# Kernel optimization log

Hardware: AMD Instinct MI355X
Metric: run time of the kernel (lower is better)

The kernel has to match this reference:

```python
import jax, jax.numpy as jnp
import numpy as np


def _euclidean_cdist(x, q):
    # torch.cdist with p=2: pairwise L2 distances, shape [B, Q]
    x2 = jnp.sum(x * x, axis=-1, keepdims=True)          # [B, 1]
    q2 = jnp.sum(q * q, axis=-1)[None, :]                # [1, Q]
    d2 = x2 + q2 - 2.0 * (x @ q.T)                        # [B, Q]
    return jnp.sqrt(jnp.maximum(d2, 0.0))


def setup_inputs() -> dict:
    key = jax.random.key(0)
    k1, k2 = jax.random.split(key)
    x = jax.random.normal(k1, (1024, 256), dtype=jnp.float32)
    queue = jax.random.normal(k2, (32768, 256), dtype=jnp.float32)
    return {"x": x, "queue": queue}


def reference(x, queue):
    # Queue update: concat then keep the newest max_size rows (queue assumed full)
    max_size = queue.shape[0]
    q = jnp.concatenate([queue, x], axis=0)[-max_size:]   # [Q, F]
    # Distance matrix + top-2 nearest (topk of negated distances)
    d = _euclidean_cdist(x, q)                            # [B, Q]
    _, idx = jax.lax.top_k(-d, 2)                         # [B, 2]
    # Second-nearest neighbor (first is the point itself, dist 0)
    return q[idx[:, 1]]                                   # [B, F]
```

## Files before the change

### kernel.cpp

```cpp
#include <hip/hip_runtime.h>
#include <stdint.h>

#define B_ROWS 1024
#define FEAT   256
#define QSZ    32768
#define SHIFT  1024
#define QX     (QSZ - B_ROWS)
#define BM     64
#define NGY    (QSZ / BM)
#define NCOL   1024
#define MARGIN 8.0f

typedef float  v4f __attribute__((ext_vector_type(4)));
typedef short  v8s __attribute__((ext_vector_type(8)));
typedef int    v4i __attribute__((ext_vector_type(4)));

#define PIN8(X)                                        \
    {                                                  \
        v4i _t = __builtin_bit_cast(v4i, X);           \
        asm volatile("" : "+v"(_t));                   \
        X = __builtin_bit_cast(v8s, _t);               \
    }

__device__ __forceinline__ uint32_t key_flip(uint32_t u) {
    return u ^ ((uint32_t)((int32_t)u >> 31) | 0x80000000u);
}
__device__ __forceinline__ float key_m(uint32_t k) {
    uint32_t u = k & 0xFFFF8000u;
    u = (u & 0x80000000u) ? (u ^ 0x80000000u) : ~u;
    return __uint_as_float(u);
}
__device__ __forceinline__ void k2_insert(uint32_t& k1, uint32_t& k2, uint32_t key) {
    uint32_t hi = max(k1, key); k1 = min(k1, key); k2 = min(k2, hi);
}
__device__ __forceinline__ uint2 k2_merge(uint2 a, uint2 b) {
    uint32_t hi = max(a.x, b.x);
    uint2 r; r.x = min(a.x, b.x); r.y = min(min(a.y, b.y), hi);
    return r;
}

struct Top2 { float m1; int j1; float m2; int j2; };
__device__ __forceinline__ bool better(float ma, int ja, float mb, int jb) {
    return (ma < mb) || (ma == mb && ja < jb);
}
__device__ __forceinline__ void t2_insert(Top2& t, float m, int j) {
    if (better(m, j, t.m1, t.j1)) { t.m2 = t.m1; t.j2 = t.j1; t.m1 = m; t.j1 = j; }
    else if (better(m, j, t.m2, t.j2)) { t.m2 = m; t.j2 = j; }
}

__device__ __forceinline__ const float* q_row_ptr(int j, const float* x, const float* queue) {
    return (j < QX) ? (queue + (size_t)(j + SHIFT) * FEAT) : (x + (size_t)(j - QX) * FEAT);
}

__device__ __forceinline__ unsigned short f2bf(float f) {
    uint32_t u = __float_as_uint(f);
    uint32_t r = u + 0x7FFFu + ((u >> 16) & 1u);
    return (unsigned short)(r >> 16);
}

__global__ __launch_bounds__(256) void convert_x(const float* __restrict__ x,
                                                 unsigned short* __restrict__ x_bf) {
    int wave = threadIdx.x >> 6, lane = threadIdx.x & 63;
    int r = blockIdx.x * 4 + wave;
    float4 v = ((const float4*)(x + (size_t)r * FEAT))[lane];
    ushort4 h;
    h.x = f2bf(v.x); h.y = f2bf(v.y); h.z = f2bf(v.z); h.w = f2bf(v.w);
    ((ushort4*)x_bf)[(size_t)r * 64 + lane] = h;
}


#define KEYI(ACC, Q2V, J)                                                  \
    {                                                                      \
        float m_ = fmaf(-2.0f, (ACC), (Q2V));                              \
        uint32_t u_ = key_flip(__float_as_uint(m_));                       \
        k2_insert(k1, k2, (u_ & 0xFFFF8000u) | (uint32_t)(J));             \
    }

#define PROCESS(TN, FB)                                                    \
    {                                                                      \
        v4f a0 = (v4f)0.0f, a1 = (v4f)0.0f, a2 = (v4f)0.0f, a3 = (v4f)0.0f;\
        __builtin_amdgcn_s_setprio(1);                                     \
        _Pragma("unroll")                                                  \
        for (int kc = 0; kc < 8; ++kc) {                                   \
            a0 = __builtin_amdgcn_mfma_f32_16x16x32_bf16(fa0[kc], FB[kc], a0, 0, 0, 0); \
            a1 = __builtin_amdgcn_mfma_f32_16x16x32_bf16(fa1[kc], FB[kc], a1, 0, 0, 0); \
            a2 = __builtin_amdgcn_mfma_f32_16x16x32_bf16(fa2[kc], FB[kc], a2, 0, 0, 0); \
            a3 = __builtin_amdgcn_mfma_f32_16x16x32_bf16(fa3[kc], FB[kc], a3, 0, 0, 0); \
        }                                                                  \
        __builtin_amdgcn_s_setprio(0);                                     \
        uint32_t k1 = 0xFFFFFFFFu, k2 = 0xFFFFFFFFu;                       \
        _Pragma("unroll")                                                  \
        for (int r = 0; r < 4; ++r) {                                      \
            KEYI(a0[r], q2r0[r], jb + 0  + r);                             \
            KEYI(a1[r], q2r1[r], jb + 16 + r);                             \
            KEYI(a2[r], q2r2[r], jb + 32 + r);                             \
            KEYI(a3[r], q2r3[r], jb + 48 + r);                             \
        }                                                                  \
        _Pragma("unroll")                                                  \
        for (int mask = 16; mask <= 32; mask <<= 1) {                      \
            uint32_t o1 = __shfl_xor(k1, mask, 64);                        \
            uint32_t o2 = __shfl_xor(k2, mask, 64);                        \
            uint32_t hi = max(k1, o1);                                     \
            k1 = min(k1, o1);                                              \
            k2 = min(min(k2, o2), hi);                                     \
        }                                                                  \
        if (quad == 0)                                                     \
            partials[(size_t)gy * NCOL + (w * 256 + (TN) * 16 + l16)] =    \
                make_uint2(k1, k2);                                        \
    }

__global__ __launch_bounds__(256, 2) void nn_gemm(const float* __restrict__ x,
                                                  const float* __restrict__ queue,
                                                  const unsigned short* __restrict__ x_bf,
                                                  float* __restrict__ q2,
                                                  uint2* __restrict__ partials) {
    __shared__ __align__(16) unsigned short As[BM * FEAT];
    __shared__ __align__(16) float sq2[BM];

    const int t    = threadIdx.x;
    const int w    = t >> 6, lane = t & 63;
    const int quad = lane >> 4, l16 = lane & 15;
    const int gy   = blockIdx.x;

    const unsigned short* bbase = x_bf + (size_t)(w * 256 + l16) * FEAT + quad * 8;
    v8s fb0[8], fb1[8];
#pragma unroll
    for (int kc = 0; kc < 8; ++kc) fb0[kc] = *(const v8s*)(bbase + kc * 32);

    {
        const int arow = t >> 2, aqtr = t & 3;
        const float* asrc = q_row_ptr(gy * BM + arow, x, queue) + aqtr * 64;
        float ss = 0.0f;
#pragma unroll
        for (int gi = 0; gi < 8; ++gi) {
            float4 a = *(const float4*)(asrc + gi * 8);
            float4 b = *(const float4*)(asrc + gi * 8 + 4);
            ss += a.x * a.x + a.y * a.y + a.z * a.z + a.w * a.w
                + b.x * b.x + b.y * b.y + b.z * b.z + b.w * b.w;
            uint32_t p0 = (uint32_t)f2bf(a.x) | ((uint32_t)f2bf(a.y) << 16);
            uint32_t p1 = (uint32_t)f2bf(a.z) | ((uint32_t)f2bf(a.w) << 16);
            uint32_t p2 = (uint32_t)f2bf(b.x) | ((uint32_t)f2bf(b.y) << 16);
            uint32_t p3 = (uint32_t)f2bf(b.z) | ((uint32_t)f2bf(b.w) << 16);
            const int g    = aqtr * 8 + gi;
            const int phys = (g & 24) | ((g & 7) ^ (arow & 7));
            *(uint4*)&As[arow * FEAT + phys * 8] = make_uint4(p0, p1, p2, p3);
        }
        ss += __shfl_xor(ss, 1, 64);
        ss += __shfl_xor(ss, 2, 64);
        if (aqtr == 0) { sq2[arow] = ss; q2[gy * BM + arow] = ss; }
    }

    __syncthreads();

    v8s fa0[8], fa1[8], fa2[8], fa3[8];
#pragma unroll
    for (int kc = 0; kc < 8; ++kc) {
        const int g  = kc * 4 + quad;
        const int pg = (g & 24) | ((g & 7) ^ (l16 & 7));
        const char* rowb = (const char*)As + (size_t)l16 * 512 + pg * 16;
        fa0[kc] = *(const v8s*)(rowb);
        fa1[kc] = *(const v8s*)(rowb + 1 * 16 * 512);
        fa2[kc] = *(const v8s*)(rowb + 2 * 16 * 512);
        fa3[kc] = *(const v8s*)(rowb + 3 * 16 * 512);
    }
#pragma unroll
    for (int kc = 0; kc < 8; ++kc) {
        PIN8(fa0[kc]); PIN8(fa1[kc]); PIN8(fa2[kc]); PIN8(fa3[kc]);
    }

    v4f q2r0 = *(const v4f*)&sq2[ 0 + quad * 4];
    v4f q2r1 = *(const v4f*)&sq2[16 + quad * 4];
    v4f q2r2 = *(const v4f*)&sq2[32 + quad * 4];
    v4f q2r3 = *(const v4f*)&sq2[48 + quad * 4];
    const int jb = gy * BM + quad * 4;

#pragma unroll
    for (int tp = 0; tp < 8; ++tp) {
        const int tn0 = tp * 2;
#pragma unroll
        for (int kc = 0; kc < 8; ++kc)
            fb1[kc] = *(const v8s*)(bbase + (size_t)(tn0 + 1) * (16 * FEAT) + kc * 32);
        PROCESS(tn0, fb0);
        if (tp < 7) {
#pragma unroll
            for (int kc = 0; kc < 8; ++kc)
                fb0[kc] = *(const v8s*)(bbase + (size_t)(tn0 + 2) * (16 * FEAT) + kc * 32);
        }
        PROCESS(tn0 + 1, fb1);
    }
}

__global__ __launch_bounds__(256) void nn_finalize(const float* __restrict__ x,
                                                   const float* __restrict__ queue,
                                                   const float* __restrict__ q2,
                                                   const uint2* __restrict__ partials,
                                                   float* __restrict__ out) {
    __shared__ float    xs[256];
    __shared__ uint2    red[256];
    __shared__ int      list[64];
    __shared__ float    escore[64];
    __shared__ int      s_cnt;
    __shared__ uint32_t s_kcut;
    __shared__ int      s_j2;

    const int t = threadIdx.x, i = blockIdx.x;
    const int w = t >> 6, lane = t & 63;

    xs[t] = x[(size_t)i * FEAT + t];
    uint2 pa = partials[(size_t)t * NCOL + i];
    uint2 pb = partials[(size_t)(t + 256) * NCOL + i];
    uint2 pm = k2_merge(pa, pb);
    red[t] = pm;
    if (t == 0) s_cnt = 0;
    __syncthreads();

    if (w == 0) {
        uint2 a = red[lane];
        a = k2_merge(a, red[lane + 64]);
        a = k2_merge(a, red[lane + 128]);
        a = k2_merge(a, red[lane + 192]);
#pragma unroll
        for (int mask = 1; mask <= 32; mask <<= 1) {
            uint2 o;
            o.x = __shfl_xor(a.x, mask, 64);
            o.y = __shfl_xor(a.y, mask, 64);
            a = k2_merge(a, o);
        }
        if (lane == 0) {
            float cutf = key_m(a.y) + MARGIN;
            s_kcut = key_flip(__float_as_uint(cutf)) | 0x7FFFu;
        }
    }
    __syncthreads();
    uint32_t kcut = s_kcut;
    if (pm.x <= kcut) { int q_ = atomicAdd(&s_cnt, 1); if (q_ < 64) list[q_] = (int)(pm.x & 0x7FFFu); }
    if (pm.y <= kcut) { int q_ = atomicAdd(&s_cnt, 1); if (q_ < 64) list[q_] = (int)(pm.y & 0x7FFFu); }
    __syncthreads();
    int n = min(s_cnt, 64);

    for (int c = w; c < n; c += 4) {
        int j = list[c];
        const float4* qr = (const float4*)q_row_ptr(j, x, queue);
        float4 qv = qr[lane];
        float4 xv = ((const float4*)xs)[lane];
        float s = qv.x * xv.x + qv.y * xv.y + qv.z * xv.z + qv.w * xv.w;
#pragma unroll
        for (int off = 32; off; off >>= 1) s += __shfl_xor(s, off, 64);
        if (lane == 0) escore[c] = q2[j] - 2.0f * s;
    }
    __syncthreads();
    if (t == 0) {
        Top2 a;
        a.m1 = __builtin_inff(); a.j1 = 0x7FFFFFFF;
        a.m2 = __builtin_inff(); a.j2 = 0x7FFFFFFF;
        for (int c = 0; c < n; ++c) t2_insert(a, escore[c], list[c]);
        s_j2 = a.j2;
    }
    __syncthreads();
    out[(size_t)i * FEAT + t] = q_row_ptr(s_j2, x, queue)[t];
}

extern "C" void kernel_launch(void* const* d_in, const int* in_sizes, int n_in,
                              void* d_out, int out_size, void* d_ws, size_t ws_size,
                              hipStream_t stream) {
    const float* x     = (const float*)d_in[0];
    const float* queue = (const float*)d_in[1];

    unsigned short* x_bf     = (unsigned short*)d_ws;
    float*          q2       = (float*)((char*)d_ws + (1u << 20));
    uint2*          partials = (uint2*)((char*)d_ws + (2u << 20));

    convert_x<<<B_ROWS / 4, 256, 0, stream>>>(x, x_bf);
    nn_gemm<<<NGY, 256, 0, stream>>>(x, queue, x_bf, q2, partials);
    nn_finalize<<<B_ROWS, 256, 0, stream>>>(x, queue, q2, partials, (float*)d_out);
}
```

Baseline: 122.0 us.

## Pre-convert whole queue to bf16 in separate pass, load A fragments from global

The queue (plus x) conversion to bf16 and its squared-norm computation move out of the GEMM kernel into a standalone convert pass over all 32768 rows. The GEMM then reads bf16 A fragments and norms directly from global memory with no LDS staging or block barrier. The partials layout is also transposed so the finalize kernel reads each query's 512 candidates contiguously. The cost is an extra 16 MB bf16 write plus re-read, in exchange for a simpler, barrier-free GEMM prologue and coalesced finalize loads.

New measurement: 128.7 us. 5.5% more time.

```diff
diff --git a/kernel.cpp b/kernel.cpp
--- a/kernel.cpp
+++ b/kernel.cpp
@@ -58,14 +58,21 @@
     return (unsigned short)(r >> 16);
 }
 
-__global__ __launch_bounds__(256) void convert_x(const float* __restrict__ x,
-                                                 unsigned short* __restrict__ x_bf) {
+__global__ __launch_bounds__(256) void convert_kernel(const float* __restrict__ x,
+                                                      const float* __restrict__ queue,
+                                                      unsigned short* __restrict__ q_bf,
+                                                      float* __restrict__ q2) {
     int wave = threadIdx.x >> 6, lane = threadIdx.x & 63;
-    int r = blockIdx.x * 4 + wave;
-    float4 v = ((const float4*)(x + (size_t)r * FEAT))[lane];
+    int j = blockIdx.x * 4 + wave;
+    const float4* row = (const float4*)q_row_ptr(j, x, queue);
+    float4 v = row[lane];
+    float s = v.x * v.x + v.y * v.y + v.z * v.z + v.w * v.w;
+#pragma unroll
+    for (int off = 32; off; off >>= 1) s += __shfl_xor(s, off, 64);
+    if (lane == 0) q2[j] = s;
     ushort4 h;
     h.x = f2bf(v.x); h.y = f2bf(v.y); h.z = f2bf(v.z); h.w = f2bf(v.w);
-    ((ushort4*)x_bf)[(size_t)r * 64 + lane] = h;
+    ((ushort4*)q_bf)[(size_t)j * 64 + lane] = h;
 }
 
 
@@ -105,73 +112,42 @@
             k2 = min(min(k2, o2), hi);                                     \
         }                                                                  \
         if (quad == 0)                                                     \
-            partials[(size_t)gy * NCOL + (w * 256 + (TN) * 16 + l16)] =    \
+            partials[(size_t)(w * 256 + (TN) * 16 + l16) * NGY + gy] =     \
                 make_uint2(k1, k2);                                        \
     }
 
-__global__ __launch_bounds__(256, 2) void nn_gemm(const float* __restrict__ x,
-                                                  const float* __restrict__ queue,
-                                                  const unsigned short* __restrict__ x_bf,
-                                                  float* __restrict__ q2,
+__global__ __launch_bounds__(256, 2) void nn_gemm(const unsigned short* __restrict__ q_bf,
+                                                  const float* __restrict__ q2,
                                                   uint2* __restrict__ partials) {
-    __shared__ __align__(16) unsigned short As[BM * FEAT];
-    __shared__ __align__(16) float sq2[BM];
-
     const int t    = threadIdx.x;
     const int w    = t >> 6, lane = t & 63;
     const int quad = lane >> 4, l16 = lane & 15;
     const int gy   = blockIdx.x;
+    const unsigned short* x_bf = q_bf + (size_t)QX * FEAT;
 
     const unsigned short* bbase = x_bf + (size_t)(w * 256 + l16) * FEAT + quad * 8;
     v8s fb0[8], fb1[8];
 #pragma unroll
     for (int kc = 0; kc < 8; ++kc) fb0[kc] = *(const v8s*)(bbase + kc * 32);
 
-    {
-        const int arow = t >> 2, aqtr = t & 3;
-        const float* asrc = q_row_ptr(gy * BM + arow, x, queue) + aqtr * 64;
-        float ss = 0.0f;
-#pragma unroll
-        for (int gi = 0; gi < 8; ++gi) {
-            float4 a = *(const float4*)(asrc + gi * 8);
-            float4 b = *(const float4*)(asrc + gi * 8 + 4);
-            ss += a.x * a.x + a.y * a.y + a.z * a.z + a.w * a.w
-                + b.x * b.x + b.y * b.y + b.z * b.z + b.w * b.w;
-            uint32_t p0 = (uint32_t)f2bf(a.x) | ((uint32_t)f2bf(a.y) << 16);
-            uint32_t p1 = (uint32_t)f2bf(a.z) | ((uint32_t)f2bf(a.w) << 16);
-            uint32_t p2 = (uint32_t)f2bf(b.x) | ((uint32_t)f2bf(b.y) << 16);
-            uint32_t p3 = (uint32_t)f2bf(b.z) | ((uint32_t)f2bf(b.w) << 16);
-            const int g    = aqtr * 8 + gi;
-            const int phys = (g & 24) | ((g & 7) ^ (arow & 7));
-            *(uint4*)&As[arow * FEAT + phys * 8] = make_uint4(p0, p1, p2, p3);
-        }
-        ss += __shfl_xor(ss, 1, 64);
-        ss += __shfl_xor(ss, 2, 64);
-        if (aqtr == 0) { sq2[arow] = ss; q2[gy * BM + arow] = ss; }
-    }
-
-    __syncthreads();
-
+    const unsigned short* abase = q_bf + (size_t)(gy * BM + l16) * FEAT + quad * 8;
     v8s fa0[8], fa1[8], fa2[8], fa3[8];
 #pragma unroll
     for (int kc = 0; kc < 8; ++kc) {
-        const int g  = kc * 4 + quad;
-        const int pg = (g & 24) | ((g & 7) ^ (l16 & 7));
-        const char* rowb = (const char*)As + (size_t)l16 * 512 + pg * 16;
-        fa0[kc] = *(const v8s*)(rowb);
-        fa1[kc] = *(const v8s*)(rowb + 1 * 16 * 512);
-        fa2[kc] = *(const v8s*)(rowb + 2 * 16 * 512);
-        fa3[kc] = *(const v8s*)(rowb + 3 * 16 * 512);
+        fa0[kc] = *(const v8s*)(abase + 0 * 16 * FEAT + kc * 32);
+        fa1[kc] = *(const v8s*)(abase + 1 * 16 * FEAT + kc * 32);
+        fa2[kc] = *(const v8s*)(abase + 2 * 16 * FEAT + kc * 32);
+        fa3[kc] = *(const v8s*)(abase + 3 * 16 * FEAT + kc * 32);
     }
 #pragma unroll
     for (int kc = 0; kc < 8; ++kc) {
         PIN8(fa0[kc]); PIN8(fa1[kc]); PIN8(fa2[kc]); PIN8(fa3[kc]);
     }
 
-    v4f q2r0 = *(const v4f*)&sq2[ 0 + quad * 4];
-    v4f q2r1 = *(const v4f*)&sq2[16 + quad * 4];
-    v4f q2r2 = *(const v4f*)&sq2[32 + quad * 4];
-    v4f q2r3 = *(const v4f*)&sq2[48 + quad * 4];
+    v4f q2r0 = *(const v4f*)(q2 + gy * BM +  0 + quad * 4);
+    v4f q2r1 = *(const v4f*)(q2 + gy * BM + 16 + quad * 4);
+    v4f q2r2 = *(const v4f*)(q2 + gy * BM + 32 + quad * 4);
+    v4f q2r3 = *(const v4f*)(q2 + gy * BM + 48 + quad * 4);
     const int jb = gy * BM + quad * 4;
 
 #pragma unroll
@@ -207,8 +183,8 @@
     const int w = t >> 6, lane = t & 63;
 
     xs[t] = x[(size_t)i * FEAT + t];
-    uint2 pa = partials[(size_t)t * NCOL + i];
-    uint2 pb = partials[(size_t)(t + 256) * NCOL + i];
+    uint2 pa = partials[(size_t)i * NGY + t];
+    uint2 pb = partials[(size_t)i * NGY + 256 + t];
     uint2 pm = k2_merge(pa, pb);
     red[t] = pm;
     if (t == 0) s_cnt = 0;
@@ -266,11 +242,11 @@
     const float* x     = (const float*)d_in[0];
     const float* queue = (const float*)d_in[1];
 
-    unsigned short* x_bf     = (unsigned short*)d_ws;
-    float*          q2       = (float*)((char*)d_ws + (1u << 20));
-    uint2*          partials = (uint2*)((char*)d_ws + (2u << 20));
-
-    convert_x<<<B_ROWS / 4, 256, 0, stream>>>(x, x_bf);
-    nn_gemm<<<NGY, 256, 0, stream>>>(x, queue, x_bf, q2, partials);
+    unsigned short* q_bf     = (unsigned short*)d_ws;
+    float*          q2       = (float*)((char*)d_ws + (16u << 20));
+    uint2*          partials = (uint2*)((char*)d_ws + (17u << 20));
+
+    convert_kernel<<<QSZ / 4, 256, 0, stream>>>(x, queue, q_bf, q2);
+    nn_gemm<<<NGY, 256, 0, stream>>>(q_bf, q2, partials);
     nn_finalize<<<B_ROWS, 256, 0, stream>>>(x, queue, q2, partials, (float*)d_out);
 }
```
